# Optimization experiments

Measured on AMD Instinct MI355X. Metric: run time of the kernel, lower is better.

The kernel has to match this reference:

```python
import jax, jax.numpy as jnp
import numpy as np

GAMMA = 0.9  # decay (init kwarg)


def setup_inputs() -> dict:
    key = jax.random.key(0)
    k0, k1, k2, k3 = jax.random.split(key, 4)
    B, T, D = 16, 2048, 256
    x = jax.random.normal(k0, (B, T, D), jnp.float32)
    scale = 1.0 / np.sqrt(D)
    Wq = jax.random.normal(k1, (D, D), jnp.float32) * scale
    Wk = jax.random.normal(k2, (D, D), jnp.float32) * scale
    Wv = jax.random.normal(k3, (D, D), jnp.float32) * scale
    return {"x": x, "Wq": Wq, "Wk": Wk, "Wv": Wv}


def reference(x, Wq, Wk, Wv):
    # x: [B, T, D]
    B, T, D = x.shape
    Q = x @ Wq  # [B, T, D]
    K = x @ Wk
    V = x @ Wv

    # Sequential retention recurrence over the [D, D] state:
    #   s[t] = gamma * s[t-1] + K[:, t, :]^T @ V[:, t, :]   (sums over batch, as in source)
    Kt = jnp.swapaxes(K, 0, 1)  # [T, B, D]
    Vt = jnp.swapaxes(V, 0, 1)  # [T, B, D]

    def step(s, kv):
        k_t, v_t = kv  # each [B, D]
        s = GAMMA * s + k_t.T @ v_t  # [D, D]
        return s, s.sum(-1)  # emit row-sum [D]

    # Loop runs t = 1 .. T-1 in the source (s starts at 0); s[0] := s[1].
    init = jnp.zeros((D, D), x.dtype)
    _, rows = jax.lax.scan(step, init, (Kt[1:], Vt[1:]))  # rows: [T-1, D]
    S = jnp.concatenate([rows[:1], rows], axis=0)  # [T, D]

    # Faithful to tf.reshape(S, [-1, seq_len]) then tf.transpose: a reshape-scramble,
    # NOT a plain transpose of S.
    S2 = S.reshape(D, T).T  # [T, D]
    return S2[None, :, :] * Q  # broadcast over batch -> [B, T, D]
```

## Files before the change

### kernel.cpp

```cpp
#include <hip/hip_runtime.h>
#include <math.h>


#define GAMMA_F 0.9f
#define T_LEN 2048
#define D_DIM 256
#define B_DIM 16

typedef __attribute__((ext_vector_type(8))) short bf16x8;
typedef __attribute__((ext_vector_type(16))) float f32x16;

__device__ inline ushort f2bf(float f) {
    union { float f; unsigned u; } v; v.f = f;
    unsigned r = (v.u + 0x7FFFu + ((v.u >> 16) & 1u)) >> 16;
    return (ushort)r;
}

__device__ __forceinline__ void gload_lds16(const void* g, void* l) {
    __builtin_amdgcn_global_load_lds(
        (const __attribute__((address_space(1))) unsigned int*)g,
        (__attribute__((address_space(3))) unsigned int*)l, 16, 0, 0);
}

__global__ __launch_bounds__(256) void k_prep(const float* __restrict__ Wq,
                                              const float* __restrict__ Wk,
                                              const float* __restrict__ Wv,
                                              ushort* __restrict__ WqT,
                                              ushort* __restrict__ WkT,
                                              float* __restrict__ wv_sum) {
    int bid = blockIdx.x;
    int tid = threadIdx.x;
    if (bid < 32) {
        __shared__ float tile[64][68];
        const float* W = (bid < 16) ? Wq : Wk;
        ushort* WT = (bid < 16) ? WqT : WkT;
        int b = bid & 15;
        int k0 = (b & 3) * 64;
        int n0 = (b >> 2) * 64;
        int r = tid >> 4;
        int c4 = (tid & 15) * 4;
#pragma unroll
        for (int i = 0; i < 4; ++i) {
            float4 v = *(const float4*)(W + (size_t)(k0 + r + 16 * i) * D_DIM + n0 + c4);
            *(float4*)&tile[r + 16 * i][c4] = v;
        }
        __syncthreads();
        int n = tid >> 2;
        int j0 = (tid & 3) * 16;
        ushort tmp[16];
#pragma unroll
        for (int i = 0; i < 16; ++i) tmp[i] = f2bf(tile[j0 + i][n]);
        ushort* dst = WT + (size_t)(n0 + n) * D_DIM + k0 + j0;
#pragma unroll
        for (int i = 0; i < 16; ++i) dst[i] = tmp[i];
    } else {
        int j = (bid - 32) * 64 + (tid >> 2);
        int q = tid & 3;
        const float4* row4 = (const float4*)(Wv + (size_t)j * D_DIM + q * 64);
        float s = 0.f;
#pragma unroll
        for (int i = 0; i < 16; ++i) {
            float4 v = row4[i];
            s += v.x + v.y + v.z + v.w;
        }
        s += __shfl_xor(s, 1, 64);
        s += __shfl_xor(s, 2, 64);
        if (q == 0) wv_sum[j] = s;
    }
}

__global__ __launch_bounds__(256) void k_y(const float* __restrict__ x,
                                           const float* __restrict__ wv_sum,
                                           ushort* __restrict__ ybf,
                                           ushort* __restrict__ xbf) {
    int tid = threadIdx.x;
    int lane = tid & 63;
    int t = blockIdx.x * 4 + (tid >> 6);
    int d0 = lane * 4;
    float4 wv4 = *(const float4*)(wv_sum + d0);

    float4 xr[B_DIM];
    float w[B_DIM];
#pragma unroll
    for (int b = 0; b < B_DIM; ++b) {
        xr[b] = *(const float4*)(x + ((size_t)b * T_LEN + t) * D_DIM + d0);
        float p = xr[b].x * wv4.x + xr[b].y * wv4.y + xr[b].z * wv4.z + xr[b].w * wv4.w;
#pragma unroll
        for (int o = 32; o > 0; o >>= 1) p += __shfl_xor(p, o, 64);
        w[b] = p;
    }

    float4 acc = make_float4(0.f, 0.f, 0.f, 0.f);
#pragma unroll
    for (int b = 0; b < B_DIM; ++b) {
        acc.x += w[b] * xr[b].x;
        acc.y += w[b] * xr[b].y;
        acc.z += w[b] * xr[b].z;
        acc.w += w[b] * xr[b].w;
        ushort4 s;
        s.x = f2bf(xr[b].x); s.y = f2bf(xr[b].y);
        s.z = f2bf(xr[b].z); s.w = f2bf(xr[b].w);
        *(ushort4*)&xbf[((size_t)b * T_LEN + t) * D_DIM + d0] = s;
    }
    ushort4 ys;
    ys.x = f2bf(acc.x); ys.y = f2bf(acc.y);
    ys.z = f2bf(acc.z); ys.w = f2bf(acc.w);
    *(ushort4*)&ybf[(size_t)t * D_DIM + d0] = ys;
}

__global__ __launch_bounds__(256) void k_gs(const ushort* __restrict__ ybf,
                                            const ushort* __restrict__ WkT,
                                            float* __restrict__ loc,
                                            float* __restrict__ carry) {
    __shared__ ushort As[32 * 64 * 8];
    __shared__ ushort Bs[32 * 64 * 8];
    float* Cs = (float*)As;
    int mt = blockIdx.x >> 2;
    int nt = blockIdx.x & 3;
    int tid = threadIdx.x, lane = tid & 63, w = tid >> 6;
    int wr = w >> 1, wc = w & 1, l31 = lane & 31, lh = lane >> 5;

#pragma unroll
    for (int i = 0; i < 8; ++i) {
        int slot = tid + 256 * i;
        int r = slot >> 5;
        int s2h = slot & 31;
        int rs = r ^ (s2h & 7);
        *(bf16x8*)&As[(s2h * 64 + rs) * 8] =
            *(const bf16x8*)&ybf[(size_t)(mt * 64 + r) * D_DIM + s2h * 8];
        *(bf16x8*)&Bs[(s2h * 64 + rs) * 8] =
            *(const bf16x8*)&WkT[(size_t)(nt * 64 + r) * D_DIM + s2h * 8];
    }
    __syncthreads();

    f32x16 acc;
#pragma unroll
    for (int e = 0; e < 16; ++e) acc[e] = 0.f;
#pragma unroll
    for (int s = 0; s < 16; ++s) {
        int s2h = s * 2 + lh;
        int ra = (wr * 32 + l31) ^ (s2h & 7);
        int rb = (wc * 32 + l31) ^ (s2h & 7);
        bf16x8 a = *(bf16x8*)&As[(s2h * 64 + ra) * 8];
        bf16x8 b = *(bf16x8*)&Bs[(s2h * 64 + rb) * 8];
        acc = __builtin_amdgcn_mfma_f32_32x32x16_bf16(a, b, acc, 0, 0, 0);
    }
    __syncthreads();

#pragma unroll
    for (int reg = 0; reg < 16; ++reg) {
        int rr = (reg & 3) + 8 * (reg >> 2) + 4 * lh;
        Cs[(wr * 32 + rr) * 64 + wc * 32 + l31] = acc[reg];
    }
    __syncthreads();

#pragma unroll
    for (int half = 0; half < 2; ++half) {
        int task = half * 256 + tid;
        int dl = task & 63;
        int cl = task >> 6;
        float a = 0.f;
#pragma unroll
        for (int j = 0; j < 8; ++j) {
            int tl = cl * 8 + j;
            int gt = mt * 64 + tl;
            float v = (gt == 0) ? 0.f : Cs[tl * 64 + dl];
            a = GAMMA_F * a + v;
            loc[(size_t)gt * D_DIM + nt * 64 + dl] = a;
        }
        carry[(size_t)(mt * 8 + cl) * D_DIM + nt * 64 + dl] = a;
    }
}

__global__ __launch_bounds__(256) void k_S2P(const float* __restrict__ loc,
                                             const float* __restrict__ carry,
                                             float* __restrict__ S2) {
    __shared__ float Ls[256][33];
    int o = blockIdx.x >> 3;
    int dseg = blockIdx.x & 7;
    int r = threadIdx.x;
    int dstart = dseg * 32;
    const float g8 = 0.43046721f;
    const float log2g = -0.15200309344504995f;
    float gp = exp2f((float)(o + 1) * log2g);

    float p = 0.f;
    int j0 = dstart - 32; if (j0 < 0) j0 = 0;
    for (int j = j0; j < dstart; ++j)
        p = p * g8 + carry[(size_t)j * D_DIM + r];

#pragma unroll
    for (int dd = 0; dd < 32; ++dd) {
        int d_ = dstart + dd;
        float Aval = loc[(size_t)(8 * d_ + o) * D_DIM + r] + gp * p;
        if (o == 0 && d_ == 0) Aval = loc[D_DIM + r];
        Ls[r][dd] = Aval;
        p = p * g8 + carry[(size_t)d_ * D_DIM + r];
    }
    __syncthreads();

    int rr = threadIdx.x >> 3;
    int cq = threadIdx.x & 7;
#pragma unroll
    for (int it = 0; it < 8; ++it) {
        int row = it * 32 + rr;
        float4 v;
        v.x = Ls[row][cq * 4 + 0];
        v.y = Ls[row][cq * 4 + 1];
        v.z = Ls[row][cq * 4 + 2];
        v.w = Ls[row][cq * 4 + 3];
        *(float4*)&S2[(size_t)((o << 8) + row) * D_DIM + dstart + cq * 4] = v;
    }
}

__global__ __launch_bounds__(256) void k_qgemm(const ushort* __restrict__ xbf,
                                               const ushort* __restrict__ WqT,
                                               const float* __restrict__ S2,
                                               float* __restrict__ out) {
    __shared__ ushort As[2][8 * 128 * 8];
    __shared__ ushort Bs[2][8 * 128 * 8];
    int bid = blockIdx.x;
    int mb = bid >> 1;
    int nb = bid & 1;
    int tid = threadIdx.x;
    int lane = tid & 63, w = tid >> 6;
    int wr = w >> 1, wc = w & 1;
    int l31 = lane & 31, lh = lane >> 5;

    f32x16 acc[2][2];
#pragma unroll
    for (int i = 0; i < 2; ++i)
#pragma unroll
        for (int j = 0; j < 2; ++j)
#pragma unroll
            for (int e = 0; e < 16; ++e) acc[i][j][e] = 0.f;

    const ushort* ab = xbf + (size_t)mb * 128 * D_DIM;
    const ushort* bb = WqT + (size_t)nb * 128 * D_DIM;

#define STAGE(buf, kb)                                                        \
    do {                                                                      \
        _Pragma("unroll")                                                     \
        for (int i = 0; i < 4; ++i) {                                         \
            int slot = i * 256 + tid;             \
            int kk = slot >> 7;                                               \
            int row = slot & 127;                                             \
            int ldsbase = (i * 256 + w * 64) * 8;      \
            gload_lds16(ab + (size_t)row * D_DIM + (kb) * 64 + kk * 8,        \
                        &As[buf][ldsbase]);                                   \
            gload_lds16(bb + (size_t)row * D_DIM + (kb) * 64 + kk * 8,        \
                        &Bs[buf][ldsbase]);                                   \
        }                                                                     \
    } while (0)

    STAGE(0, 0);
    __syncthreads();

#pragma unroll
    for (int kb = 0; kb < 4; ++kb) {
        int cur = kb & 1;
        if (kb < 3) STAGE(cur ^ 1, kb + 1);
#pragma unroll
        for (int s = 0; s < 4; ++s) {
            int c0 = (s * 2 + lh) * 128;
            bf16x8 a0 = *(bf16x8*)&As[cur][(c0 + wr * 64 + l31) * 8];
            bf16x8 a1 = *(bf16x8*)&As[cur][(c0 + wr * 64 + 32 + l31) * 8];
            bf16x8 b0 = *(bf16x8*)&Bs[cur][(c0 + wc * 64 + l31) * 8];
            bf16x8 b1 = *(bf16x8*)&Bs[cur][(c0 + wc * 64 + 32 + l31) * 8];
            acc[0][0] = __builtin_amdgcn_mfma_f32_32x32x16_bf16(a0, b0, acc[0][0], 0, 0, 0);
            acc[0][1] = __builtin_amdgcn_mfma_f32_32x32x16_bf16(a0, b1, acc[0][1], 0, 0, 0);
            acc[1][0] = __builtin_amdgcn_mfma_f32_32x32x16_bf16(a1, b0, acc[1][0], 0, 0, 0);
            acc[1][1] = __builtin_amdgcn_mfma_f32_32x32x16_bf16(a1, b1, acc[1][1], 0, 0, 0);
        }
        if (kb < 3) __syncthreads();
    }
#undef STAGE

    int t_base = (mb & 15) * 128;
    size_t row_base = (size_t)mb * 128;
#pragma unroll
    for (int mi = 0; mi < 2; ++mi) {
#pragma unroll
        for (int ni = 0; ni < 2; ++ni) {
            int gn = nb * 128 + wc * 64 + ni * 32 + l31;
#pragma unroll
            for (int reg = 0; reg < 16; ++reg) {
                int rr = (reg & 3) + 8 * (reg >> 2) + 4 * lh;
                int m = wr * 64 + mi * 32 + rr;
                float s2v = S2[(size_t)(t_base + m) * D_DIM + gn];
                out[(row_base + m) * D_DIM + gn] = acc[mi][ni][reg] * s2v;
            }
        }
    }
}

extern "C" void kernel_launch(void* const* d_in, const int* in_sizes, int n_in,
                              void* d_out, int out_size, void* d_ws, size_t ws_size,
                              hipStream_t stream) {
    const float* x  = (const float*)d_in[0];
    const float* Wq = (const float*)d_in[1];
    const float* Wk = (const float*)d_in[2];
    const float* Wv = (const float*)d_in[3];
    float* out = (float*)d_out;

    float* ws = (float*)d_ws;
    float* loc    = ws;
    float* S2     = loc + 524288;
    float* wv_sum = S2 + 524288;
    float* carry  = wv_sum + 256;
    ushort* WqT   = (ushort*)(carry + 65536);
    ushort* WkT   = WqT + 65536;
    ushort* ybf   = WkT + 65536;
    ushort* xbf   = ybf + 524288;

    k_prep<<<36, 256, 0, stream>>>(Wq, Wk, Wv, WqT, WkT, wv_sum);
    k_y<<<T_LEN / 4, 256, 0, stream>>>(x, wv_sum, ybf, xbf);
    k_gs<<<128, 256, 0, stream>>>(ybf, WkT, loc, carry);
    k_S2P<<<64, 256, 0, stream>>>(loc, carry, S2);
    k_qgemm<<<(B_DIM * T_LEN / 128) * 2, 256, 0, stream>>>(xbf, WqT, S2, out);
}
```

Before: 122.5 us.

## Fuse five kernels into one persistent kernel with atomic grid barriers

Replaces the five separate launches (prep, y, gs, S2P, qgemm) with a single 256-block persistent kernel. Stages are separated by software grid barriers built on an atomic counter, which a tiny init kernel resets. Each block now redundantly recomputes the Wv row sums into LDS instead of reading them from a separate pass. The aim is to cut launch and inter-kernel gap overhead, at the cost of spin-wait barriers, idle blocks in the smaller stages, and reliance on all 256 blocks being co-resident.

```diff
diff --git a/kernel.cpp b/kernel.cpp
--- a/kernel.cpp
+++ b/kernel.cpp
@@ -22,221 +22,237 @@
         (__attribute__((address_space(3))) unsigned int*)l, 16, 0, 0);
 }
 
-__global__ __launch_bounds__(256) void k_prep(const float* __restrict__ Wq,
-                                              const float* __restrict__ Wk,
-                                              const float* __restrict__ Wv,
-                                              ushort* __restrict__ WqT,
-                                              ushort* __restrict__ WkT,
-                                              float* __restrict__ wv_sum) {
+__device__ __forceinline__ void grid_sync(unsigned* cnt, unsigned target, int tid) {
+    __threadfence();
+    __syncthreads();
+    if (tid == 0) {
+        __hip_atomic_fetch_add(cnt, 1u, __ATOMIC_ACQ_REL, __HIP_MEMORY_SCOPE_AGENT);
+        while (__hip_atomic_load(cnt, __ATOMIC_ACQUIRE, __HIP_MEMORY_SCOPE_AGENT) < target)
+            __builtin_amdgcn_s_sleep(2);
+    }
+    __syncthreads();
+    __threadfence();
+}
+
+__global__ void k_init(unsigned* cnt) { *cnt = 0u; }
+
+__global__ __launch_bounds__(256) void k_fused(const float* __restrict__ x,
+                                               const float* __restrict__ Wq,
+                                               const float* __restrict__ Wk,
+                                               const float* __restrict__ Wv,
+                                               float* __restrict__ out,
+                                               float* __restrict__ ws) {
+    float* loc    = ws;
+    float* S2     = loc + 524288;
+    float* carry  = S2 + 524288 + 256;
+    ushort* WqT   = (ushort*)(carry + 65536);
+    ushort* WkT   = WqT + 65536;
+    ushort* ybf   = WkT + 65536;
+    ushort* xbf   = ybf + 524288;
+    unsigned* cnt = (unsigned*)(ws + 6815744);
+
+    __shared__ char LDSBUF[65536] __attribute__((aligned(128)));
+
     int bid = blockIdx.x;
     int tid = threadIdx.x;
-    if (bid < 32) {
-        __shared__ float tile[64][68];
-        const float* W = (bid < 16) ? Wq : Wk;
-        ushort* WT = (bid < 16) ? WqT : WkT;
-        int b = bid & 15;
-        int k0 = (b & 3) * 64;
-        int n0 = (b >> 2) * 64;
-        int r = tid >> 4;
-        int c4 = (tid & 15) * 4;
-#pragma unroll
-        for (int i = 0; i < 4; ++i) {
-            float4 v = *(const float4*)(W + (size_t)(k0 + r + 16 * i) * D_DIM + n0 + c4);
-            *(float4*)&tile[r + 16 * i][c4] = v;
-        }
-        __syncthreads();
-        int n = tid >> 2;
-        int j0 = (tid & 3) * 16;
-        ushort tmp[16];
-#pragma unroll
-        for (int i = 0; i < 16; ++i) tmp[i] = f2bf(tile[j0 + i][n]);
-        ushort* dst = WT + (size_t)(n0 + n) * D_DIM + k0 + j0;
-#pragma unroll
-        for (int i = 0; i < 16; ++i) dst[i] = tmp[i];
-    } else {
-        int j = (bid - 32) * 64 + (tid >> 2);
-        int q = tid & 3;
-        const float4* row4 = (const float4*)(Wv + (size_t)j * D_DIM + q * 64);
-        float s = 0.f;
-#pragma unroll
-        for (int i = 0; i < 16; ++i) {
-            float4 v = row4[i];
-            s += v.x + v.y + v.z + v.w;
-        }
-        s += __shfl_xor(s, 1, 64);
-        s += __shfl_xor(s, 2, 64);
-        if (q == 0) wv_sum[j] = s;
-    }
-}
-
-__global__ __launch_bounds__(256) void k_y(const float* __restrict__ x,
-                                           const float* __restrict__ wv_sum,
-                                           ushort* __restrict__ ybf,
-                                           ushort* __restrict__ xbf) {
-    int tid = threadIdx.x;
-    int lane = tid & 63;
-    int t = blockIdx.x * 4 + (tid >> 6);
-    int d0 = lane * 4;
-    float4 wv4 = *(const float4*)(wv_sum + d0);
-
-    float4 xr[B_DIM];
-    float w[B_DIM];
-#pragma unroll
-    for (int b = 0; b < B_DIM; ++b) {
-        xr[b] = *(const float4*)(x + ((size_t)b * T_LEN + t) * D_DIM + d0);
-        float p = xr[b].x * wv4.x + xr[b].y * wv4.y + xr[b].z * wv4.z + xr[b].w * wv4.w;
-#pragma unroll
-        for (int o = 32; o > 0; o >>= 1) p += __shfl_xor(p, o, 64);
-        w[b] = p;
-    }
-
-    float4 acc = make_float4(0.f, 0.f, 0.f, 0.f);
-#pragma unroll
-    for (int b = 0; b < B_DIM; ++b) {
-        acc.x += w[b] * xr[b].x;
-        acc.y += w[b] * xr[b].y;
-        acc.z += w[b] * xr[b].z;
-        acc.w += w[b] * xr[b].w;
-        ushort4 s;
-        s.x = f2bf(xr[b].x); s.y = f2bf(xr[b].y);
-        s.z = f2bf(xr[b].z); s.w = f2bf(xr[b].w);
-        *(ushort4*)&xbf[((size_t)b * T_LEN + t) * D_DIM + d0] = s;
-    }
-    ushort4 ys;
-    ys.x = f2bf(acc.x); ys.y = f2bf(acc.y);
-    ys.z = f2bf(acc.z); ys.w = f2bf(acc.w);
-    *(ushort4*)&ybf[(size_t)t * D_DIM + d0] = ys;
-}
-
-__global__ __launch_bounds__(256) void k_gs(const ushort* __restrict__ ybf,
-                                            const ushort* __restrict__ WkT,
-                                            float* __restrict__ loc,
-                                            float* __restrict__ carry) {
-    __shared__ ushort As[32 * 64 * 8];
-    __shared__ ushort Bs[32 * 64 * 8];
-    float* Cs = (float*)As;
-    int mt = blockIdx.x >> 2;
-    int nt = blockIdx.x & 3;
-    int tid = threadIdx.x, lane = tid & 63, w = tid >> 6;
-    int wr = w >> 1, wc = w & 1, l31 = lane & 31, lh = lane >> 5;
-
-#pragma unroll
-    for (int i = 0; i < 8; ++i) {
-        int slot = tid + 256 * i;
-        int r = slot >> 5;
-        int s2h = slot & 31;
-        int rs = r ^ (s2h & 7);
-        *(bf16x8*)&As[(s2h * 64 + rs) * 8] =
-            *(const bf16x8*)&ybf[(size_t)(mt * 64 + r) * D_DIM + s2h * 8];
-        *(bf16x8*)&Bs[(s2h * 64 + rs) * 8] =
-            *(const bf16x8*)&WkT[(size_t)(nt * 64 + r) * D_DIM + s2h * 8];
-    }
-    __syncthreads();
-
-    f32x16 acc;
-#pragma unroll
-    for (int e = 0; e < 16; ++e) acc[e] = 0.f;
-#pragma unroll
-    for (int s = 0; s < 16; ++s) {
-        int s2h = s * 2 + lh;
-        int ra = (wr * 32 + l31) ^ (s2h & 7);
-        int rb = (wc * 32 + l31) ^ (s2h & 7);
-        bf16x8 a = *(bf16x8*)&As[(s2h * 64 + ra) * 8];
-        bf16x8 b = *(bf16x8*)&Bs[(s2h * 64 + rb) * 8];
-        acc = __builtin_amdgcn_mfma_f32_32x32x16_bf16(a, b, acc, 0, 0, 0);
-    }
-    __syncthreads();
-
-#pragma unroll
-    for (int reg = 0; reg < 16; ++reg) {
-        int rr = (reg & 3) + 8 * (reg >> 2) + 4 * lh;
-        Cs[(wr * 32 + rr) * 64 + wc * 32 + l31] = acc[reg];
-    }
-    __syncthreads();
-
-#pragma unroll
-    for (int half = 0; half < 2; ++half) {
-        int task = half * 256 + tid;
-        int dl = task & 63;
-        int cl = task >> 6;
-        float a = 0.f;
-#pragma unroll
-        for (int j = 0; j < 8; ++j) {
-            int tl = cl * 8 + j;
-            int gt = mt * 64 + tl;
-            float v = (gt == 0) ? 0.f : Cs[tl * 64 + dl];
-            a = GAMMA_F * a + v;
-            loc[(size_t)gt * D_DIM + nt * 64 + dl] = a;
-        }
-        carry[(size_t)(mt * 8 + cl) * D_DIM + nt * 64 + dl] = a;
-    }
-}
-
-__global__ __launch_bounds__(256) void k_S2P(const float* __restrict__ loc,
-                                             const float* __restrict__ carry,
-                                             float* __restrict__ S2) {
-    __shared__ float Ls[256][33];
-    int o = blockIdx.x >> 3;
-    int dseg = blockIdx.x & 7;
-    int r = threadIdx.x;
-    int dstart = dseg * 32;
-    const float g8 = 0.43046721f;
-    const float log2g = -0.15200309344504995f;
-    float gp = exp2f((float)(o + 1) * log2g);
-
-    float p = 0.f;
-    int j0 = dstart - 32; if (j0 < 0) j0 = 0;
-    for (int j = j0; j < dstart; ++j)
-        p = p * g8 + carry[(size_t)j * D_DIM + r];
-
-#pragma unroll
-    for (int dd = 0; dd < 32; ++dd) {
-        int d_ = dstart + dd;
-        float Aval = loc[(size_t)(8 * d_ + o) * D_DIM + r] + gp * p;
-        if (o == 0 && d_ == 0) Aval = loc[D_DIM + r];
-        Ls[r][dd] = Aval;
-        p = p * g8 + carry[(size_t)d_ * D_DIM + r];
-    }
-    __syncthreads();
-
-    int rr = threadIdx.x >> 3;
-    int cq = threadIdx.x & 7;
-#pragma unroll
-    for (int it = 0; it < 8; ++it) {
-        int row = it * 32 + rr;
-        float4 v;
-        v.x = Ls[row][cq * 4 + 0];
-        v.y = Ls[row][cq * 4 + 1];
-        v.z = Ls[row][cq * 4 + 2];
-        v.w = Ls[row][cq * 4 + 3];
-        *(float4*)&S2[(size_t)((o << 8) + row) * D_DIM + dstart + cq * 4] = v;
-    }
-}
-
-__global__ __launch_bounds__(256) void k_qgemm(const ushort* __restrict__ xbf,
-                                               const ushort* __restrict__ WqT,
-                                               const float* __restrict__ S2,
-                                               float* __restrict__ out) {
-    __shared__ ushort As[2][8 * 128 * 8];
-    __shared__ ushort Bs[2][8 * 128 * 8];
-    int bid = blockIdx.x;
-    int mb = bid >> 1;
-    int nb = bid & 1;
-    int tid = threadIdx.x;
-    int lane = tid & 63, w = tid >> 6;
-    int wr = w >> 1, wc = w & 1;
-    int l31 = lane & 31, lh = lane >> 5;
-
-    f32x16 acc[2][2];
-#pragma unroll
-    for (int i = 0; i < 2; ++i)
-#pragma unroll
-        for (int j = 0; j < 2; ++j)
-#pragma unroll
-            for (int e = 0; e < 16; ++e) acc[i][j][e] = 0.f;
-
-    const ushort* ab = xbf + (size_t)mb * 128 * D_DIM;
-    const ushort* bb = WqT + (size_t)nb * 128 * D_DIM;
+    int lane = tid & 63, wave = tid >> 6;
+
+    {
+        float* wv = (float*)LDSBUF;
+        {
+            const float4* row4 = (const float4*)(Wv + (size_t)tid * D_DIM);
+            float s = 0.f;
+#pragma unroll 8
+            for (int i = 0; i < 64; ++i) {
+                float4 v = row4[i];
+                s += v.x + v.y + v.z + v.w;
+            }
+            wv[tid] = s;
+        }
+        __syncthreads();
+        int d0 = lane * 4;
+        float4 wv4 = *(float4*)&wv[d0];
+
+#pragma unroll
+        for (int j = 0; j < 2; ++j) {
+            int t = bid * 8 + wave * 2 + j;
+            float4 xr[B_DIM];
+            float w_[B_DIM];
+#pragma unroll
+            for (int b = 0; b < B_DIM; ++b) {
+                xr[b] = *(const float4*)(x + ((size_t)b * T_LEN + t) * D_DIM + d0);
+                float p = xr[b].x * wv4.x + xr[b].y * wv4.y +
+                          xr[b].z * wv4.z + xr[b].w * wv4.w;
+#pragma unroll
+                for (int o = 32; o > 0; o >>= 1) p += __shfl_xor(p, o, 64);
+                w_[b] = p;
+            }
+            float4 acc = make_float4(0.f, 0.f, 0.f, 0.f);
+#pragma unroll
+            for (int b = 0; b < B_DIM; ++b) {
+                acc.x += w_[b] * xr[b].x;
+                acc.y += w_[b] * xr[b].y;
+                acc.z += w_[b] * xr[b].z;
+                acc.w += w_[b] * xr[b].w;
+                ushort4 sx;
+                sx.x = f2bf(xr[b].x); sx.y = f2bf(xr[b].y);
+                sx.z = f2bf(xr[b].z); sx.w = f2bf(xr[b].w);
+                *(ushort4*)&xbf[((size_t)b * T_LEN + t) * D_DIM + d0] = sx;
+            }
+            ushort4 ys;
+            ys.x = f2bf(acc.x); ys.y = f2bf(acc.y);
+            ys.z = f2bf(acc.z); ys.w = f2bf(acc.w);
+            *(ushort4*)&ybf[(size_t)t * D_DIM + d0] = ys;
+        }
+
+        if (bid < 32) {
+            float (*tile)[68] = (float(*)[68])(LDSBUF + 2048);
+            const float* W = (bid < 16) ? Wq : Wk;
+            ushort* WT = (bid < 16) ? WqT : WkT;
+            int b = bid & 15;
+            int k0 = (b & 3) * 64;
+            int n0 = (b >> 2) * 64;
+            int r = tid >> 4;
+            int c4 = (tid & 15) * 4;
+#pragma unroll
+            for (int i = 0; i < 4; ++i) {
+                float4 v = *(const float4*)(W + (size_t)(k0 + r + 16 * i) * D_DIM + n0 + c4);
+                *(float4*)&tile[r + 16 * i][c4] = v;
+            }
+            __syncthreads();
+            int n = tid >> 2;
+            int j0 = (tid & 3) * 16;
+            ushort tmp[16];
+#pragma unroll
+            for (int i = 0; i < 16; ++i) tmp[i] = f2bf(tile[j0 + i][n]);
+            ushort* dst = WT + (size_t)(n0 + n) * D_DIM + k0 + j0;
+#pragma unroll
+            for (int i = 0; i < 16; ++i) dst[i] = tmp[i];
+        }
+    }
+    grid_sync(cnt, 256, tid);
+
+    if (bid < 128) {
+        ushort* As = (ushort*)LDSBUF;
+        ushort* Bs = (ushort*)(LDSBUF + 32768);
+        float* Cs = (float*)LDSBUF;
+        int mt = bid >> 2;
+        int nt = bid & 3;
+        int wr = wave >> 1, wc = wave & 1, l31 = lane & 31, lh = lane >> 5;
+
+#pragma unroll
+        for (int i = 0; i < 8; ++i) {
+            int slot = tid + 256 * i;
+            int r = slot >> 5;
+            int s2h = slot & 31;
+            int rs = r ^ (s2h & 7);
+            *(bf16x8*)&As[(s2h * 64 + rs) * 8] =
+                *(const bf16x8*)&ybf[(size_t)(mt * 64 + r) * D_DIM + s2h * 8];
+            *(bf16x8*)&Bs[(s2h * 64 + rs) * 8] =
+                *(const bf16x8*)&WkT[(size_t)(nt * 64 + r) * D_DIM + s2h * 8];
+        }
+        __syncthreads();
+
+        f32x16 acc;
+#pragma unroll
+        for (int e = 0; e < 16; ++e) acc[e] = 0.f;
+#pragma unroll
+        for (int s = 0; s < 16; ++s) {
+            int s2h = s * 2 + lh;
+            int ra = (wr * 32 + l31) ^ (s2h & 7);
+            int rb = (wc * 32 + l31) ^ (s2h & 7);
+            bf16x8 a = *(bf16x8*)&As[(s2h * 64 + ra) * 8];
+            bf16x8 b = *(bf16x8*)&Bs[(s2h * 64 + rb) * 8];
+            acc = __builtin_amdgcn_mfma_f32_32x32x16_bf16(a, b, acc, 0, 0, 0);
+        }
+        __syncthreads();
+
+#pragma unroll
+        for (int reg = 0; reg < 16; ++reg) {
+            int rr = (reg & 3) + 8 * (reg >> 2) + 4 * lh;
+            Cs[(wr * 32 + rr) * 64 + wc * 32 + l31] = acc[reg];
+        }
+        __syncthreads();
+
+#pragma unroll
+        for (int half = 0; half < 2; ++half) {
+            int task = half * 256 + tid;
+            int dl = task & 63;
+            int cl = task >> 6;
+            float a = 0.f;
+#pragma unroll
+            for (int j = 0; j < 8; ++j) {
+                int tl = cl * 8 + j;
+                int gt = mt * 64 + tl;
+                float v = (gt == 0) ? 0.f : Cs[tl * 64 + dl];
+                a = GAMMA_F * a + v;
+                loc[(size_t)gt * D_DIM + nt * 64 + dl] = a;
+            }
+            carry[(size_t)(mt * 8 + cl) * D_DIM + nt * 64 + dl] = a;
+        }
+    }
+    grid_sync(cnt, 512, tid);
+
+    if (bid < 64) {
+        float (*Ls)[33] = (float(*)[33])LDSBUF;
+        int o = bid >> 3;
+        int dseg = bid & 7;
+        int r = tid;
+        int dstart = dseg * 32;
+        const float g8 = 0.43046721f;
+        const float log2g = -0.15200309344504995f;
+        float gp = exp2f((float)(o + 1) * log2g);
+
+        float p = 0.f;
+        int j0 = dstart - 32; if (j0 < 0) j0 = 0;
+        for (int j = j0; j < dstart; ++j)
+            p = p * g8 + carry[(size_t)j * D_DIM + r];
+
+#pragma unroll
+        for (int dd = 0; dd < 32; ++dd) {
+            int d_ = dstart + dd;
+            float Aval = loc[(size_t)(8 * d_ + o) * D_DIM + r] + gp * p;
+            if (o == 0 && d_ == 0) Aval = loc[D_DIM + r];
+            Ls[r][dd] = Aval;
+            p = p * g8 + carry[(size_t)d_ * D_DIM + r];
+        }
+        __syncthreads();
+
+        int rr = tid >> 3;
+        int cq = tid & 7;
+#pragma unroll
+        for (int it = 0; it < 8; ++it) {
+            int row = it * 32 + rr;
+            float4 v;
+            v.x = Ls[row][cq * 4 + 0];
+            v.y = Ls[row][cq * 4 + 1];
+            v.z = Ls[row][cq * 4 + 2];
+            v.w = Ls[row][cq * 4 + 3];
+            *(float4*)&S2[(size_t)((o << 8) + row) * D_DIM + dstart + cq * 4] = v;
+        }
+    }
+    grid_sync(cnt, 768, tid);
+
+    {
+        ushort (*As)[8 * 128 * 8] = (ushort(*)[8 * 128 * 8])LDSBUF;
+        ushort (*Bs)[8 * 128 * 8] = (ushort(*)[8 * 128 * 8])(LDSBUF + 32768);
+        int wr = wave >> 1, wc = wave & 1, l31 = lane & 31, lh = lane >> 5;
+
+        for (int rep = 0; rep < 2; ++rep) {
+            int v = bid + rep * 256;
+            int mb = v >> 1;
+            int nb = v & 1;
+
+            f32x16 acc[2][2];
+#pragma unroll
+            for (int i = 0; i < 2; ++i)
+#pragma unroll
+                for (int j = 0; j < 2; ++j)
+#pragma unroll
+                    for (int e = 0; e < 16; ++e) acc[i][j][e] = 0.f;
+
+            const ushort* ab = xbf + (size_t)mb * 128 * D_DIM;
+            const ushort* bb = WqT + (size_t)nb * 128 * D_DIM;
 
 #define STAGE(buf, kb)                                                        \
     do {                                                                      \
@@ -245,7 +261,7 @@
             int slot = i * 256 + tid;             \
             int kk = slot >> 7;                                               \
             int row = slot & 127;                                             \
-            int ldsbase = (i * 256 + w * 64) * 8;      \
+            int ldsbase = (i * 256 + wave * 64) * 8;   \
             gload_lds16(ab + (size_t)row * D_DIM + (kb) * 64 + kk * 8,        \
                         &As[buf][ldsbase]);                                   \
             gload_lds16(bb + (size_t)row * D_DIM + (kb) * 64 + kk * 8,        \
@@ -253,42 +269,45 @@
         }                                                                     \
     } while (0)
 
-    STAGE(0, 0);
-    __syncthreads();
-
-#pragma unroll
-    for (int kb = 0; kb < 4; ++kb) {
-        int cur = kb & 1;
-        if (kb < 3) STAGE(cur ^ 1, kb + 1);
-#pragma unroll
-        for (int s = 0; s < 4; ++s) {
-            int c0 = (s * 2 + lh) * 128;
-            bf16x8 a0 = *(bf16x8*)&As[cur][(c0 + wr * 64 + l31) * 8];
-            bf16x8 a1 = *(bf16x8*)&As[cur][(c0 + wr * 64 + 32 + l31) * 8];
-            bf16x8 b0 = *(bf16x8*)&Bs[cur][(c0 + wc * 64 + l31) * 8];
-            bf16x8 b1 = *(bf16x8*)&Bs[cur][(c0 + wc * 64 + 32 + l31) * 8];
-            acc[0][0] = __builtin_amdgcn_mfma_f32_32x32x16_bf16(a0, b0, acc[0][0], 0, 0, 0);
-            acc[0][1] = __builtin_amdgcn_mfma_f32_32x32x16_bf16(a0, b1, acc[0][1], 0, 0, 0);
-            acc[1][0] = __builtin_amdgcn_mfma_f32_32x32x16_bf16(a1, b0, acc[1][0], 0, 0, 0);
-            acc[1][1] = __builtin_amdgcn_mfma_f32_32x32x16_bf16(a1, b1, acc[1][1], 0, 0, 0);
-        }
-        if (kb < 3) __syncthreads();
-    }
+            __syncthreads();
+            STAGE(0, 0);
+            __syncthreads();
+
+#pragma unroll
+            for (int kb = 0; kb < 4; ++kb) {
+                int cur = kb & 1;
+                if (kb < 3) STAGE(cur ^ 1, kb + 1);
+#pragma unroll
+                for (int s = 0; s < 4; ++s) {
+                    int c0 = (s * 2 + lh) * 128;
+                    bf16x8 a0 = *(bf16x8*)&As[cur][(c0 + wr * 64 + l31) * 8];
+                    bf16x8 a1 = *(bf16x8*)&As[cur][(c0 + wr * 64 + 32 + l31) * 8];
+                    bf16x8 b0 = *(bf16x8*)&Bs[cur][(c0 + wc * 64 + l31) * 8];
+                    bf16x8 b1 = *(bf16x8*)&Bs[cur][(c0 + wc * 64 + 32 + l31) * 8];
+                    acc[0][0] = __builtin_amdgcn_mfma_f32_32x32x16_bf16(a0, b0, acc[0][0], 0, 0, 0);
+                    acc[0][1] = __builtin_amdgcn_mfma_f32_32x32x16_bf16(a0, b1, acc[0][1], 0, 0, 0);
+                    acc[1][0] = __builtin_amdgcn_mfma_f32_32x32x16_bf16(a1, b0, acc[1][0], 0, 0, 0);
+                    acc[1][1] = __builtin_amdgcn_mfma_f32_32x32x16_bf16(a1, b1, acc[1][1], 0, 0, 0);
+                }
+                if (kb < 3) __syncthreads();
+            }
 #undef STAGE
 
-    int t_base = (mb & 15) * 128;
-    size_t row_base = (size_t)mb * 128;
-#pragma unroll
-    for (int mi = 0; mi < 2; ++mi) {
-#pragma unroll
-        for (int ni = 0; ni < 2; ++ni) {
-            int gn = nb * 128 + wc * 64 + ni * 32 + l31;
-#pragma unroll
-            for (int reg = 0; reg < 16; ++reg) {
-                int rr = (reg & 3) + 8 * (reg >> 2) + 4 * lh;
-                int m = wr * 64 + mi * 32 + rr;
-                float s2v = S2[(size_t)(t_base + m) * D_DIM + gn];
-                out[(row_base + m) * D_DIM + gn] = acc[mi][ni][reg] * s2v;
+            int t_base = (mb & 15) * 128;
+            size_t row_base = (size_t)mb * 128;
+#pragma unroll
+            for (int mi = 0; mi < 2; ++mi) {
+#pragma unroll
+                for (int ni = 0; ni < 2; ++ni) {
+                    int gn = nb * 128 + wc * 64 + ni * 32 + l31;
+#pragma unroll
+                    for (int reg = 0; reg < 16; ++reg) {
+                        int rr = (reg & 3) + 8 * (reg >> 2) + 4 * lh;
+                        int m = wr * 64 + mi * 32 + rr;
+                        float s2v = S2[(size_t)(t_base + m) * D_DIM + gn];
+                        out[(row_base + m) * D_DIM + gn] = acc[mi][ni][reg] * s2v;
+                    }
+                }
             }
         }
     }
@@ -302,20 +321,9 @@
     const float* Wk = (const float*)d_in[2];
     const float* Wv = (const float*)d_in[3];
     float* out = (float*)d_out;
-
     float* ws = (float*)d_ws;
-    float* loc    = ws;
-    float* S2     = loc + 524288;
-    float* wv_sum = S2 + 524288;
-    float* carry  = wv_sum + 256;
-    ushort* WqT   = (ushort*)(carry + 65536);
-    ushort* WkT   = WqT + 65536;
-    ushort* ybf   = WkT + 65536;
-    ushort* xbf   = ybf + 524288;
-
-    k_prep<<<36, 256, 0, stream>>>(Wq, Wk, Wv, WqT, WkT, wv_sum);
-    k_y<<<T_LEN / 4, 256, 0, stream>>>(x, wv_sum, ybf, xbf);
-    k_gs<<<128, 256, 0, stream>>>(ybf, WkT, loc, carry);
-    k_S2P<<<64, 256, 0, stream>>>(loc, carry, S2);
-    k_qgemm<<<(B_DIM * T_LEN / 128) * 2, 256, 0, stream>>>(xbf, WqT, S2, out);
-}
+    unsigned* cnt = (unsigned*)(ws + 6815744);
+
+    k_init<<<1, 1, 0, stream>>>(cnt);
+    k_fused<<<256, 256, 0, stream>>>(x, Wq, Wk, Wv, out, ws);
+}
```

Result: slower. 324.6 us (+165.1%).

## Fuse chunk GEMM and carry-propagation kernels with an atomic grid barrier

Applied to the files above, without the earlier changes.

Merges the chunked K-projection/local-scan kernel and the S2 assembly kernel into one launch. An atomic-counter grid barrier separates the phases, and the counter is reset in the prep kernel. The serial carry prefix loop becomes an unrolled weighted sum. This removes one kernel launch and its gap, but relies on all 128 blocks being co-resident and adds spin-wait cost.

```diff
diff --git a/kernel.cpp b/kernel.cpp
--- a/kernel.cpp
+++ b/kernel.cpp
@@ -20,6 +20,18 @@
     __builtin_amdgcn_global_load_lds(
         (const __attribute__((address_space(1))) unsigned int*)g,
         (__attribute__((address_space(3))) unsigned int*)l, 16, 0, 0);
+}
+
+__device__ __forceinline__ void grid_sync(unsigned* cnt, unsigned target, int tid) {
+    __threadfence();
+    __syncthreads();
+    if (tid == 0) {
+        __hip_atomic_fetch_add(cnt, 1u, __ATOMIC_ACQ_REL, __HIP_MEMORY_SCOPE_AGENT);
+        while (__hip_atomic_load(cnt, __ATOMIC_ACQUIRE, __HIP_MEMORY_SCOPE_AGENT) < target)
+            __builtin_amdgcn_s_sleep(2);
+    }
+    __syncthreads();
+    __threadfence();
 }
 
 __global__ __launch_bounds__(256) void k_prep(const float* __restrict__ Wq,
@@ -27,9 +39,11 @@
                                               const float* __restrict__ Wv,
                                               ushort* __restrict__ WqT,
                                               ushort* __restrict__ WkT,
-                                              float* __restrict__ wv_sum) {
+                                              float* __restrict__ wv_sum,
+                                              unsigned* __restrict__ cnt) {
     int bid = blockIdx.x;
     int tid = threadIdx.x;
+    if (bid == 0 && tid == 0) *cnt = 0u;
     if (bid < 32) {
         __shared__ float tile[64][68];
         const float* W = (bid < 16) ? Wq : Wk;
@@ -108,108 +122,121 @@
     *(ushort4*)&ybf[(size_t)t * D_DIM + d0] = ys;
 }
 
-__global__ __launch_bounds__(256) void k_gs(const ushort* __restrict__ ybf,
-                                            const ushort* __restrict__ WkT,
-                                            float* __restrict__ loc,
-                                            float* __restrict__ carry) {
-    __shared__ ushort As[32 * 64 * 8];
-    __shared__ ushort Bs[32 * 64 * 8];
-    float* Cs = (float*)As;
-    int mt = blockIdx.x >> 2;
-    int nt = blockIdx.x & 3;
+__global__ __launch_bounds__(256) void k_gs_s2p(const ushort* __restrict__ ybf,
+                                                const ushort* __restrict__ WkT,
+                                                float* __restrict__ loc,
+                                                float* __restrict__ carry,
+                                                float* __restrict__ S2,
+                                                unsigned* __restrict__ cnt) {
+    __shared__ char LDSBUF[65536] __attribute__((aligned(128)));
+    ushort* As = (ushort*)LDSBUF;
+    ushort* Bs = (ushort*)(LDSBUF + 32768);
+    float* Cs = (float*)LDSBUF;
+    int bid = blockIdx.x;
     int tid = threadIdx.x, lane = tid & 63, w = tid >> 6;
-    int wr = w >> 1, wc = w & 1, l31 = lane & 31, lh = lane >> 5;
-
-#pragma unroll
-    for (int i = 0; i < 8; ++i) {
-        int slot = tid + 256 * i;
-        int r = slot >> 5;
-        int s2h = slot & 31;
-        int rs = r ^ (s2h & 7);
-        *(bf16x8*)&As[(s2h * 64 + rs) * 8] =
-            *(const bf16x8*)&ybf[(size_t)(mt * 64 + r) * D_DIM + s2h * 8];
-        *(bf16x8*)&Bs[(s2h * 64 + rs) * 8] =
-            *(const bf16x8*)&WkT[(size_t)(nt * 64 + r) * D_DIM + s2h * 8];
-    }
-    __syncthreads();
-
-    f32x16 acc;
-#pragma unroll
-    for (int e = 0; e < 16; ++e) acc[e] = 0.f;
-#pragma unroll
-    for (int s = 0; s < 16; ++s) {
-        int s2h = s * 2 + lh;
-        int ra = (wr * 32 + l31) ^ (s2h & 7);
-        int rb = (wc * 32 + l31) ^ (s2h & 7);
-        bf16x8 a = *(bf16x8*)&As[(s2h * 64 + ra) * 8];
-        bf16x8 b = *(bf16x8*)&Bs[(s2h * 64 + rb) * 8];
-        acc = __builtin_amdgcn_mfma_f32_32x32x16_bf16(a, b, acc, 0, 0, 0);
-    }
-    __syncthreads();
-
-#pragma unroll
-    for (int reg = 0; reg < 16; ++reg) {
-        int rr = (reg & 3) + 8 * (reg >> 2) + 4 * lh;
-        Cs[(wr * 32 + rr) * 64 + wc * 32 + l31] = acc[reg];
-    }
-    __syncthreads();
-
-#pragma unroll
-    for (int half = 0; half < 2; ++half) {
-        int task = half * 256 + tid;
-        int dl = task & 63;
-        int cl = task >> 6;
-        float a = 0.f;
-#pragma unroll
-        for (int j = 0; j < 8; ++j) {
-            int tl = cl * 8 + j;
-            int gt = mt * 64 + tl;
-            float v = (gt == 0) ? 0.f : Cs[tl * 64 + dl];
-            a = GAMMA_F * a + v;
-            loc[(size_t)gt * D_DIM + nt * 64 + dl] = a;
-        }
-        carry[(size_t)(mt * 8 + cl) * D_DIM + nt * 64 + dl] = a;
-    }
-}
-
-__global__ __launch_bounds__(256) void k_S2P(const float* __restrict__ loc,
-                                             const float* __restrict__ carry,
-                                             float* __restrict__ S2) {
-    __shared__ float Ls[256][33];
-    int o = blockIdx.x >> 3;
-    int dseg = blockIdx.x & 7;
-    int r = threadIdx.x;
-    int dstart = dseg * 32;
-    const float g8 = 0.43046721f;
-    const float log2g = -0.15200309344504995f;
-    float gp = exp2f((float)(o + 1) * log2g);
-
-    float p = 0.f;
-    int j0 = dstart - 32; if (j0 < 0) j0 = 0;
-    for (int j = j0; j < dstart; ++j)
-        p = p * g8 + carry[(size_t)j * D_DIM + r];
-
-#pragma unroll
-    for (int dd = 0; dd < 32; ++dd) {
-        int d_ = dstart + dd;
-        float Aval = loc[(size_t)(8 * d_ + o) * D_DIM + r] + gp * p;
-        if (o == 0 && d_ == 0) Aval = loc[D_DIM + r];
-        Ls[r][dd] = Aval;
-        p = p * g8 + carry[(size_t)d_ * D_DIM + r];
-    }
-    __syncthreads();
-
-    int rr = threadIdx.x >> 3;
-    int cq = threadIdx.x & 7;
-#pragma unroll
-    for (int it = 0; it < 8; ++it) {
-        int row = it * 32 + rr;
-        float4 v;
-        v.x = Ls[row][cq * 4 + 0];
-        v.y = Ls[row][cq * 4 + 1];
-        v.z = Ls[row][cq * 4 + 2];
-        v.w = Ls[row][cq * 4 + 3];
-        *(float4*)&S2[(size_t)((o << 8) + row) * D_DIM + dstart + cq * 4] = v;
+
+    {
+        int mt = bid >> 2;
+        int nt = bid & 3;
+        int wr = w >> 1, wc = w & 1, l31 = lane & 31, lh = lane >> 5;
+
+#pragma unroll
+        for (int i = 0; i < 8; ++i) {
+            int slot = tid + 256 * i;
+            int r = slot >> 5;
+            int s2h = slot & 31;
+            int rs = r ^ (s2h & 7);
+            *(bf16x8*)&As[(s2h * 64 + rs) * 8] =
+                *(const bf16x8*)&ybf[(size_t)(mt * 64 + r) * D_DIM + s2h * 8];
+            *(bf16x8*)&Bs[(s2h * 64 + rs) * 8] =
+                *(const bf16x8*)&WkT[(size_t)(nt * 64 + r) * D_DIM + s2h * 8];
+        }
+        __syncthreads();
+
+        f32x16 acc;
+#pragma unroll
+        for (int e = 0; e < 16; ++e) acc[e] = 0.f;
+#pragma unroll
+        for (int s = 0; s < 16; ++s) {
+            int s2h = s * 2 + lh;
+            int ra = (wr * 32 + l31) ^ (s2h & 7);
+            int rb = (wc * 32 + l31) ^ (s2h & 7);
+            bf16x8 a = *(bf16x8*)&As[(s2h * 64 + ra) * 8];
+            bf16x8 b = *(bf16x8*)&Bs[(s2h * 64 + rb) * 8];
+            acc = __builtin_amdgcn_mfma_f32_32x32x16_bf16(a, b, acc, 0, 0, 0);
+        }
+        __syncthreads();
+
+#pragma unroll
+        for (int reg = 0; reg < 16; ++reg) {
+            int rr = (reg & 3) + 8 * (reg >> 2) + 4 * lh;
+            Cs[(wr * 32 + rr) * 64 + wc * 32 + l31] = acc[reg];
+        }
+        __syncthreads();
+
+#pragma unroll
+        for (int half = 0; half < 2; ++half) {
+            int task = half * 256 + tid;
+            int dl = task & 63;
+            int cl = task >> 6;
+            float a = 0.f;
+#pragma unroll
+            for (int j = 0; j < 8; ++j) {
+                int tl = cl * 8 + j;
+                int gt = mt * 64 + tl;
+                float v = (gt == 0) ? 0.f : Cs[tl * 64 + dl];
+                a = GAMMA_F * a + v;
+                loc[(size_t)gt * D_DIM + nt * 64 + dl] = a;
+            }
+            carry[(size_t)(mt * 8 + cl) * D_DIM + nt * 64 + dl] = a;
+        }
+    }
+
+    grid_sync(cnt, 128, tid);
+
+    if (bid < 64) {
+        float (*Ls)[33] = (float(*)[33])LDSBUF;
+        int o = bid >> 3;
+        int dseg = bid & 7;
+        int r = tid;
+        int dstart = dseg * 32;
+        const float g8 = 0.43046721f;
+        const float log2g = -0.15200309344504995f;
+        float gp = exp2f((float)(o + 1) * log2g);
+
+        float p = 0.f;
+        {
+            float wgt = 1.f;
+#pragma unroll
+            for (int i = 1; i <= 32; ++i) {
+                if (dstart - i >= 0)
+                    p += wgt * carry[(size_t)(dstart - i) * D_DIM + r];
+                wgt *= g8;
+            }
+        }
+
+#pragma unroll
+        for (int dd = 0; dd < 32; ++dd) {
+            int d_ = dstart + dd;
+            float Aval = loc[(size_t)(8 * d_ + o) * D_DIM + r] + gp * p;
+            if (o == 0 && d_ == 0) Aval = loc[D_DIM + r];
+            Ls[r][dd] = Aval;
+            p = p * g8 + carry[(size_t)d_ * D_DIM + r];
+        }
+        __syncthreads();
+
+        int rr = tid >> 3;
+        int cq = tid & 7;
+#pragma unroll
+        for (int it = 0; it < 8; ++it) {
+            int row = it * 32 + rr;
+            float4 v;
+            v.x = Ls[row][cq * 4 + 0];
+            v.y = Ls[row][cq * 4 + 1];
+            v.z = Ls[row][cq * 4 + 2];
+            v.w = Ls[row][cq * 4 + 3];
+            *(float4*)&S2[(size_t)((o << 8) + row) * D_DIM + dstart + cq * 4] = v;
+        }
     }
 }
 
@@ -312,10 +339,10 @@
     ushort* WkT   = WqT + 65536;
     ushort* ybf   = WkT + 65536;
     ushort* xbf   = ybf + 524288;
-
-    k_prep<<<36, 256, 0, stream>>>(Wq, Wk, Wv, WqT, WkT, wv_sum);
+    unsigned* cnt = (unsigned*)(ws + 6815744);
+
+    k_prep<<<36, 256, 0, stream>>>(Wq, Wk, Wv, WqT, WkT, wv_sum, cnt);
     k_y<<<T_LEN / 4, 256, 0, stream>>>(x, wv_sum, ybf, xbf);
-    k_gs<<<128, 256, 0, stream>>>(ybf, WkT, loc, carry);
-    k_S2P<<<64, 256, 0, stream>>>(loc, carry, S2);
+    k_gs_s2p<<<128, 256, 0, stream>>>(ybf, WkT, loc, carry, S2, cnt);
     k_qgemm<<<(B_DIM * T_LEN / 128) * 2, 256, 0, stream>>>(xbf, WqT, S2, out);
 }
```

After: 142.7 us. +16.6%, slower.

## Fuse S2 scramble/prefix kernel into Q-GEMM epilogue via shared memory

Applied to the files above, without the earlier changes.

Removes the separate k_S2P kernel and recomputes each block's 128x128 tile of the scrambled state (loc plus decayed carry prefix) inside the Q-GEMM epilogue. The tile is staged in the reused GEMM shared memory with an XOR swizzle, then multiplied into the accumulators. This drops one launch and the S2 global write and read-back. The cost is that each of the 512 GEMM blocks redoes the 32-step carry prefix and loc gathers, which is 16x redundant across batch.

```diff
diff --git a/kernel.cpp b/kernel.cpp
--- a/kernel.cpp
+++ b/kernel.cpp
@@ -172,53 +172,12 @@
     }
 }
 
-__global__ __launch_bounds__(256) void k_S2P(const float* __restrict__ loc,
-                                             const float* __restrict__ carry,
-                                             float* __restrict__ S2) {
-    __shared__ float Ls[256][33];
-    int o = blockIdx.x >> 3;
-    int dseg = blockIdx.x & 7;
-    int r = threadIdx.x;
-    int dstart = dseg * 32;
-    const float g8 = 0.43046721f;
-    const float log2g = -0.15200309344504995f;
-    float gp = exp2f((float)(o + 1) * log2g);
-
-    float p = 0.f;
-    int j0 = dstart - 32; if (j0 < 0) j0 = 0;
-    for (int j = j0; j < dstart; ++j)
-        p = p * g8 + carry[(size_t)j * D_DIM + r];
-
-#pragma unroll
-    for (int dd = 0; dd < 32; ++dd) {
-        int d_ = dstart + dd;
-        float Aval = loc[(size_t)(8 * d_ + o) * D_DIM + r] + gp * p;
-        if (o == 0 && d_ == 0) Aval = loc[D_DIM + r];
-        Ls[r][dd] = Aval;
-        p = p * g8 + carry[(size_t)d_ * D_DIM + r];
-    }
-    __syncthreads();
-
-    int rr = threadIdx.x >> 3;
-    int cq = threadIdx.x & 7;
-#pragma unroll
-    for (int it = 0; it < 8; ++it) {
-        int row = it * 32 + rr;
-        float4 v;
-        v.x = Ls[row][cq * 4 + 0];
-        v.y = Ls[row][cq * 4 + 1];
-        v.z = Ls[row][cq * 4 + 2];
-        v.w = Ls[row][cq * 4 + 3];
-        *(float4*)&S2[(size_t)((o << 8) + row) * D_DIM + dstart + cq * 4] = v;
-    }
-}
-
 __global__ __launch_bounds__(256) void k_qgemm(const ushort* __restrict__ xbf,
                                                const ushort* __restrict__ WqT,
-                                               const float* __restrict__ S2,
+                                               const float* __restrict__ loc,
+                                               const float* __restrict__ carry,
                                                float* __restrict__ out) {
-    __shared__ ushort As[2][8 * 128 * 8];
-    __shared__ ushort Bs[2][8 * 128 * 8];
+    __shared__ char QL[65536] __attribute__((aligned(128)));
     int bid = blockIdx.x;
     int mb = bid >> 1;
     int nb = bid & 1;
@@ -238,6 +197,8 @@
     const ushort* ab = xbf + (size_t)mb * 128 * D_DIM;
     const ushort* bb = WqT + (size_t)nb * 128 * D_DIM;
 
+#define ASP(buf) ((ushort*)(QL + (buf) * 16384))
+#define BSP(buf) ((ushort*)(QL + 32768 + (buf) * 16384))
 #define STAGE(buf, kb)                                                        \
     do {                                                                      \
         _Pragma("unroll")                                                     \
@@ -247,9 +208,9 @@
             int row = slot & 127;                                             \
             int ldsbase = (i * 256 + w * 64) * 8;      \
             gload_lds16(ab + (size_t)row * D_DIM + (kb) * 64 + kk * 8,        \
-                        &As[buf][ldsbase]);                                   \
+                        ASP(buf) + ldsbase);                                  \
             gload_lds16(bb + (size_t)row * D_DIM + (kb) * 64 + kk * 8,        \
-                        &Bs[buf][ldsbase]);                                   \
+                        BSP(buf) + ldsbase);                                  \
         }                                                                     \
     } while (0)
 
@@ -263,10 +224,10 @@
 #pragma unroll
         for (int s = 0; s < 4; ++s) {
             int c0 = (s * 2 + lh) * 128;
-            bf16x8 a0 = *(bf16x8*)&As[cur][(c0 + wr * 64 + l31) * 8];
-            bf16x8 a1 = *(bf16x8*)&As[cur][(c0 + wr * 64 + 32 + l31) * 8];
-            bf16x8 b0 = *(bf16x8*)&Bs[cur][(c0 + wc * 64 + l31) * 8];
-            bf16x8 b1 = *(bf16x8*)&Bs[cur][(c0 + wc * 64 + 32 + l31) * 8];
+            bf16x8 a0 = *(bf16x8*)&ASP(cur)[(c0 + wr * 64 + l31) * 8];
+            bf16x8 a1 = *(bf16x8*)&ASP(cur)[(c0 + wr * 64 + 32 + l31) * 8];
+            bf16x8 b0 = *(bf16x8*)&BSP(cur)[(c0 + wc * 64 + l31) * 8];
+            bf16x8 b1 = *(bf16x8*)&BSP(cur)[(c0 + wc * 64 + 32 + l31) * 8];
             acc[0][0] = __builtin_amdgcn_mfma_f32_32x32x16_bf16(a0, b0, acc[0][0], 0, 0, 0);
             acc[0][1] = __builtin_amdgcn_mfma_f32_32x32x16_bf16(a0, b1, acc[0][1], 0, 0, 0);
             acc[1][0] = __builtin_amdgcn_mfma_f32_32x32x16_bf16(a1, b0, acc[1][0], 0, 0, 0);
@@ -275,20 +236,58 @@
         if (kb < 3) __syncthreads();
     }
 #undef STAGE
-
-    int t_base = (mb & 15) * 128;
+#undef ASP
+#undef BSP
+
+    __syncthreads();
+
+    float* Ls = (float*)QL;
+    {
+        int rloc = tid & 127;
+        int h = tid >> 7;
+        int rglob = (mb & 1) * 128 + rloc;
+        int o = (mb & 15) >> 1;
+        int gn0 = nb * 128;
+        int gstart = gn0 + h * 64;
+        const float g8 = 0.43046721f;
+        const float log2g = -0.15200309344504995f;
+        float gpo = exp2f((float)(o + 1) * log2g);
+
+        float p = 0.f;
+        if (gstart > 0) {
+            float wgt = 1.f;
+#pragma unroll
+            for (int i = 1; i <= 32; ++i) {
+                p += wgt * carry[(size_t)(gstart - i) * D_DIM + rglob];
+                wgt *= g8;
+            }
+        }
+#pragma unroll 8
+        for (int gl = 0; gl < 64; ++gl) {
+            int gn = gstart + gl;
+            float locv = loc[(size_t)(8 * gn + o) * D_DIM + rglob];
+            float Av = fmaf(gpo, p, locv);
+            if (o == 0 && gn == 0) Av = loc[D_DIM + rglob];
+            int gnl = gn - gn0;
+            Ls[rloc * 128 + (gnl ^ (rloc & 31))] = Av;
+            p = p * g8 + carry[(size_t)gn * D_DIM + rglob];
+        }
+    }
+    __syncthreads();
+
     size_t row_base = (size_t)mb * 128;
 #pragma unroll
     for (int mi = 0; mi < 2; ++mi) {
 #pragma unroll
         for (int ni = 0; ni < 2; ++ni) {
-            int gn = nb * 128 + wc * 64 + ni * 32 + l31;
+            int gnl = wc * 64 + ni * 32 + l31;
+            int gn_out = nb * 128 + gnl;
 #pragma unroll
             for (int reg = 0; reg < 16; ++reg) {
                 int rr = (reg & 3) + 8 * (reg >> 2) + 4 * lh;
                 int m = wr * 64 + mi * 32 + rr;
-                float s2v = S2[(size_t)(t_base + m) * D_DIM + gn];
-                out[(row_base + m) * D_DIM + gn] = acc[mi][ni][reg] * s2v;
+                float av = Ls[m * 128 + (gnl ^ (m & 31))];
+                out[(row_base + m) * D_DIM + gn_out] = acc[mi][ni][reg] * av;
             }
         }
     }
@@ -305,8 +304,8 @@
 
     float* ws = (float*)d_ws;
     float* loc    = ws;
-    float* S2     = loc + 524288;
-    float* wv_sum = S2 + 524288;
+    float* wv_sum = ws + 1048576 + 256 - 256;
+    wv_sum = ws + 1048576;
     float* carry  = wv_sum + 256;
     ushort* WqT   = (ushort*)(carry + 65536);
     ushort* WkT   = WqT + 65536;
@@ -316,6 +315,5 @@
     k_prep<<<36, 256, 0, stream>>>(Wq, Wk, Wv, WqT, WkT, wv_sum);
     k_y<<<T_LEN / 4, 256, 0, stream>>>(x, wv_sum, ybf, xbf);
     k_gs<<<128, 256, 0, stream>>>(ybf, WkT, loc, carry);
-    k_S2P<<<64, 256, 0, stream>>>(loc, carry, S2);
-    k_qgemm<<<(B_DIM * T_LEN / 128) * 2, 256, 0, stream>>>(xbf, WqT, S2, out);
-}
+    k_qgemm<<<(B_DIM * T_LEN / 128) * 2, 256, 0, stream>>>(xbf, WqT, loc, carry, out);
+}
```

Result: faster. 116.1 us (-5.2%).
